# Performance work log

Measured on AMD Instinct MI355X. Metric: run time of the kernel, lower is better.

The kernel has to match this reference:

```python
import jax, jax.numpy as jnp
import numpy as np

B, T, D_Q, D_K, D_W = 128, 4096, 16, 16, 32


def setup_inputs() -> dict:
    key0 = jax.random.key(0)
    ks = jax.random.split(key0, 8)
    return {
        "query": jax.random.normal(ks[0], (B, 1, D_Q), dtype=jnp.float32),
        "key": jax.random.normal(ks[1], (B, T, D_K), dtype=jnp.float32),
        "value": jax.random.normal(ks[2], (B, T, D_K), dtype=jnp.float32),
        "W1": jax.random.normal(ks[3], (D_W, D_Q), dtype=jnp.float32) * 0.1,
        "W2": jax.random.normal(ks[4], (D_W, D_K), dtype=jnp.float32) * 0.1,
        "bias": jax.random.uniform(ks[5], (), dtype=jnp.float32, minval=-0.1, maxval=0.1),
        "v_w": jax.random.normal(ks[6], (1, D_W), dtype=jnp.float32) * 0.1,
        "v_b": jax.random.normal(ks[7], (1,), dtype=jnp.float32) * 0.1,
    }


def reference(query, key, value, W1, W2, bias, v_w, v_b):
    # Bahdanau additive attention.
    # query: [B,1,d_q], key/value: [B,T,d_k]
    q_proj = jnp.einsum('bqd,wd->bqw', query, W1)      # [B,1,d_w]
    k_proj = jnp.einsum('btd,wd->btw', key, W2)        # [B,T,d_w]
    h = jnp.tanh(k_proj + q_proj + bias)               # [B,T,d_w]
    score = (jnp.einsum('btw,ow->bto', h, v_w) + v_b).squeeze(-1)  # [B,T]
    attn = jax.nn.softmax(score, axis=-1)              # [B,T]
    context = jnp.einsum('bt,btd->bd', attn, value)[:, None, :]    # [B,1,d_v]
    return context, attn
```

## Files before the change

kernel.cpp:

```cpp
#include <hip/hip_runtime.h>

#define NB 128
#define NT 4096
#define DKD 16
#define DW 32
#define CHUNKS 4
#define TC 1024
#define BLK 256
#define PT 4

__device__ __forceinline__ float fast_tanh(float x) {
    float e = __expf(2.0f * x);
    return 1.0f - 2.0f * __builtin_amdgcn_rcpf(e + 1.0f);
}

__global__ __launch_bounds__(BLK, 2) void aa_score(
    const float* __restrict__ query, const float* __restrict__ key,
    const float* __restrict__ value, const float* __restrict__ W1,
    const float* __restrict__ W2, const float* __restrict__ bias,
    const float* __restrict__ v_w, const float* __restrict__ v_b,
    float* __restrict__ attn,
    float* __restrict__ ws_l,
    float* __restrict__ ws_ctx)
{
    const int b   = blockIdx.x >> 2;
    const int c   = blockIdx.x & (CHUNKS - 1);
    const int tid = threadIdx.x;

    __shared__ float2 s_cv[DW];
    __shared__ float s_rctx[4 * 16];
    __shared__ float s_rl[4];

    if (tid < DW) {
        float acc = bias[0];
        const float* q  = query + b * DKD;
        const float* wr = W1 + tid * DKD;
        #pragma unroll
        for (int d = 0; d < DKD; ++d) acc = fmaf(q[d], wr[d], acc);
        s_cv[tid] = make_float2(acc, v_w[tid]);
    }
    __syncthreads();

    const float vb = v_b[0];
    const size_t tbase = (size_t)b * NT + (size_t)c * TC + (size_t)tid * PT;
    const float4* kp = reinterpret_cast<const float4*>(key)   + tbase * 4;
    const float4* vp = reinterpret_cast<const float4*>(value) + tbase * 4;

    float4 k0[PT], k1[PT], k2[PT], k3[PT];
    float4 v0[PT], v1[PT], v2[PT], v3[PT];
    #pragma unroll
    for (int j = 0; j < PT; ++j) {
        k0[j] = kp[4*j + 0]; k1[j] = kp[4*j + 1];
        k2[j] = kp[4*j + 2]; k3[j] = kp[4*j + 3];
    }
    #pragma unroll
    for (int j = 0; j < PT; ++j) {
        v0[j] = vp[4*j + 0]; v1[j] = vp[4*j + 1];
        v2[j] = vp[4*j + 2]; v3[j] = vp[4*j + 3];
    }

    float sc[PT];
    #pragma unroll
    for (int j = 0; j < PT; ++j) sc[j] = vb;

    #pragma unroll 4
    for (int w = 0; w < DW; ++w) {
        const float4* wrow = reinterpret_cast<const float4*>(W2 + w * DKD);
        const float4 u0 = wrow[0], u1 = wrow[1], u2 = wrow[2], u3 = wrow[3];
        const float2 cv = s_cv[w];
        #pragma unroll
        for (int j = 0; j < PT; ++j) {
            float h = cv.x;
            h = fmaf(k0[j].x, u0.x, h); h = fmaf(k0[j].y, u0.y, h);
            h = fmaf(k0[j].z, u0.z, h); h = fmaf(k0[j].w, u0.w, h);
            h = fmaf(k1[j].x, u1.x, h); h = fmaf(k1[j].y, u1.y, h);
            h = fmaf(k1[j].z, u1.z, h); h = fmaf(k1[j].w, u1.w, h);
            h = fmaf(k2[j].x, u2.x, h); h = fmaf(k2[j].y, u2.y, h);
            h = fmaf(k2[j].z, u2.z, h); h = fmaf(k2[j].w, u2.w, h);
            h = fmaf(k3[j].x, u3.x, h); h = fmaf(k3[j].y, u3.y, h);
            h = fmaf(k3[j].z, u3.z, h); h = fmaf(k3[j].w, u3.w, h);
            sc[j] = fmaf(fast_tanh(h), cv.y, sc[j]);
        }
    }

    float l = 0.0f;
    float ctx[16];
    #pragma unroll
    for (int d = 0; d < 16; ++d) ctx[d] = 0.0f;

    float p[PT];
    #pragma unroll
    for (int j = 0; j < PT; ++j) {
        p[j] = __expf(sc[j]);
        l += p[j];
        ctx[ 0] = fmaf(p[j], v0[j].x, ctx[ 0]); ctx[ 1] = fmaf(p[j], v0[j].y, ctx[ 1]);
        ctx[ 2] = fmaf(p[j], v0[j].z, ctx[ 2]); ctx[ 3] = fmaf(p[j], v0[j].w, ctx[ 3]);
        ctx[ 4] = fmaf(p[j], v1[j].x, ctx[ 4]); ctx[ 5] = fmaf(p[j], v1[j].y, ctx[ 5]);
        ctx[ 6] = fmaf(p[j], v1[j].z, ctx[ 6]); ctx[ 7] = fmaf(p[j], v1[j].w, ctx[ 7]);
        ctx[ 8] = fmaf(p[j], v2[j].x, ctx[ 8]); ctx[ 9] = fmaf(p[j], v2[j].y, ctx[ 9]);
        ctx[10] = fmaf(p[j], v2[j].z, ctx[10]); ctx[11] = fmaf(p[j], v2[j].w, ctx[11]);
        ctx[12] = fmaf(p[j], v3[j].x, ctx[12]); ctx[13] = fmaf(p[j], v3[j].y, ctx[13]);
        ctx[14] = fmaf(p[j], v3[j].z, ctx[14]); ctx[15] = fmaf(p[j], v3[j].w, ctx[15]);
    }

    reinterpret_cast<float4*>(attn + (size_t)b * NT + (size_t)c * TC)[tid] =
        make_float4(p[0], p[1], p[2], p[3]);

    #pragma unroll
    for (int o = 32; o > 0; o >>= 1) l += __shfl_xor(l, o);
    #pragma unroll
    for (int d = 0; d < 16; ++d) {
        #pragma unroll
        for (int o = 32; o > 0; o >>= 1) ctx[d] += __shfl_xor(ctx[d], o);
    }
    const int wave = tid >> 6;
    const int lane = tid & 63;
    if (lane == 0) {
        s_rl[wave] = l;
        #pragma unroll
        for (int d = 0; d < 16; ++d) s_rctx[wave * 16 + d] = ctx[d];
    }
    __syncthreads();
    const int slot = b * CHUNKS + c;
    if (tid < 16)
        ws_ctx[slot * 16 + tid] =
            s_rctx[tid] + s_rctx[16 + tid] + s_rctx[32 + tid] + s_rctx[48 + tid];
    if (tid == 0)
        ws_l[slot] = s_rl[0] + s_rl[1] + s_rl[2] + s_rl[3];
}

__global__ __launch_bounds__(BLK) void aa_finish(
    float* __restrict__ out,
    const float* __restrict__ ws_l,
    const float* __restrict__ ws_ctx)
{
    const int b   = blockIdx.x >> 2;
    const int q   = blockIdx.x & 3;
    const int tid = threadIdx.x;

    float L = 0.0f;
    #pragma unroll
    for (int i = 0; i < CHUNKS; ++i) L += ws_l[b * CHUNKS + i];
    const float inv = 1.0f / L;

    float4* ap = reinterpret_cast<float4*>(out + NB * DKD + (size_t)b * NT) +
                 q * BLK + tid;
    float4 p = *ap;
    p.x *= inv; p.y *= inv; p.z *= inv; p.w *= inv;
    *ap = p;

    if (q == 0 && tid < DKD) {
        const float* wc = ws_ctx + b * CHUNKS * 16;
        float s = 0.0f;
        #pragma unroll
        for (int i = 0; i < CHUNKS; ++i) s += wc[i * 16 + tid];
        out[b * DKD + tid] = s * inv;
    }
}

extern "C" void kernel_launch(void* const* d_in, const int* in_sizes, int n_in,
                              void* d_out, int out_size, void* d_ws, size_t ws_size,
                              hipStream_t stream) {
    const float* query = (const float*)d_in[0];
    const float* key   = (const float*)d_in[1];
    const float* value = (const float*)d_in[2];
    const float* W1    = (const float*)d_in[3];
    const float* W2    = (const float*)d_in[4];
    const float* bias  = (const float*)d_in[5];
    const float* v_w   = (const float*)d_in[6];
    const float* v_b   = (const float*)d_in[7];
    float* out = (float*)d_out;

    float* ws_l   = (float*)d_ws;
    float* ws_ctx = ws_l + NB * CHUNKS;

    aa_score<<<NB * CHUNKS, BLK, 0, stream>>>(
        query, key, value, W1, W2, bias, v_w, v_b,
        out + NB * DKD, ws_l, ws_ctx);
    aa_finish<<<NB * (NT / 4 / BLK), BLK, 0, stream>>>(out, ws_l, ws_ctx);
}
```

Before: 122.0 us.

## Double-buffer key/value rows and process one timestep per stage

Replaces the upfront load of all four timesteps' key/value rows with a two-slot register double buffer. Each timestep is scored fully on its own, with the next slot's loads issued behind a sched_barrier, and the 16-term dot product is split into four partial sums to shorten the dependency chain. The aim is to cut register pressure and overlap global loads with tanh/FMA compute. In exchange, the four timesteps no longer share each W2 row load across an inner loop, so W2 rows are reloaded per timestep.

Measured after the change: 123.1 us. About the same (+0.9%).

```diff
diff --git a/kernel.cpp b/kernel.cpp
--- a/kernel.cpp
+++ b/kernel.cpp
@@ -13,6 +13,42 @@
     float e = __expf(2.0f * x);
     return 1.0f - 2.0f * __builtin_amdgcn_rcpf(e + 1.0f);
 }
+
+
+#define SCORE_STAGE(K0, K1, K2, K3, X0, X1, X2, X3, POUT)                     \
+    do {                                                                      \
+        float sc_ = vb;                                                       \
+        _Pragma("unroll 8")                                                   \
+        for (int w = 0; w < DW; ++w) {                                        \
+            const float4* wr_ = reinterpret_cast<const float4*>(W2) + w * 4;  \
+            const float4 u0 = wr_[0], u1 = wr_[1], u2 = wr_[2], u3 = wr_[3];  \
+            const float2 cv_ = s_cv[w];                                       \
+            float h0 = fmaf(K0.x, u0.x, cv_.x);                               \
+            h0 = fmaf(K0.y, u0.y, h0); h0 = fmaf(K0.z, u0.z, h0);             \
+            h0 = fmaf(K0.w, u0.w, h0);                                        \
+            float h1 = K1.x * u1.x;                                           \
+            h1 = fmaf(K1.y, u1.y, h1); h1 = fmaf(K1.z, u1.z, h1);             \
+            h1 = fmaf(K1.w, u1.w, h1);                                        \
+            float h2 = K2.x * u2.x;                                           \
+            h2 = fmaf(K2.y, u2.y, h2); h2 = fmaf(K2.z, u2.z, h2);             \
+            h2 = fmaf(K2.w, u2.w, h2);                                        \
+            float h3 = K3.x * u3.x;                                           \
+            h3 = fmaf(K3.y, u3.y, h3); h3 = fmaf(K3.z, u3.z, h3);             \
+            h3 = fmaf(K3.w, u3.w, h3);                                        \
+            const float h_ = (h0 + h1) + (h2 + h3);                           \
+            sc_ = fmaf(fast_tanh(h_), cv_.y, sc_);                            \
+        }                                                                     \
+        POUT = __expf(sc_);                                                   \
+        l += POUT;                                                            \
+        ctx[ 0] = fmaf(POUT, X0.x, ctx[ 0]); ctx[ 1] = fmaf(POUT, X0.y, ctx[ 1]); \
+        ctx[ 2] = fmaf(POUT, X0.z, ctx[ 2]); ctx[ 3] = fmaf(POUT, X0.w, ctx[ 3]); \
+        ctx[ 4] = fmaf(POUT, X1.x, ctx[ 4]); ctx[ 5] = fmaf(POUT, X1.y, ctx[ 5]); \
+        ctx[ 6] = fmaf(POUT, X1.z, ctx[ 6]); ctx[ 7] = fmaf(POUT, X1.w, ctx[ 7]); \
+        ctx[ 8] = fmaf(POUT, X2.x, ctx[ 8]); ctx[ 9] = fmaf(POUT, X2.y, ctx[ 9]); \
+        ctx[10] = fmaf(POUT, X2.z, ctx[10]); ctx[11] = fmaf(POUT, X2.w, ctx[11]); \
+        ctx[12] = fmaf(POUT, X3.x, ctx[12]); ctx[13] = fmaf(POUT, X3.y, ctx[13]); \
+        ctx[14] = fmaf(POUT, X3.z, ctx[14]); ctx[15] = fmaf(POUT, X3.w, ctx[15]); \
+    } while (0)
 
 __global__ __launch_bounds__(BLK, 2) void aa_score(
     const float* __restrict__ query, const float* __restrict__ key,
@@ -46,65 +82,34 @@
     const float4* kp = reinterpret_cast<const float4*>(key)   + tbase * 4;
     const float4* vp = reinterpret_cast<const float4*>(value) + tbase * 4;
 
-    float4 k0[PT], k1[PT], k2[PT], k3[PT];
-    float4 v0[PT], v1[PT], v2[PT], v3[PT];
-    #pragma unroll
-    for (int j = 0; j < PT; ++j) {
-        k0[j] = kp[4*j + 0]; k1[j] = kp[4*j + 1];
-        k2[j] = kp[4*j + 2]; k3[j] = kp[4*j + 3];
-    }
-    #pragma unroll
-    for (int j = 0; j < PT; ++j) {
-        v0[j] = vp[4*j + 0]; v1[j] = vp[4*j + 1];
-        v2[j] = vp[4*j + 2]; v3[j] = vp[4*j + 3];
-    }
-
-    float sc[PT];
-    #pragma unroll
-    for (int j = 0; j < PT; ++j) sc[j] = vb;
-
-    #pragma unroll 4
-    for (int w = 0; w < DW; ++w) {
-        const float4* wrow = reinterpret_cast<const float4*>(W2 + w * DKD);
-        const float4 u0 = wrow[0], u1 = wrow[1], u2 = wrow[2], u3 = wrow[3];
-        const float2 cv = s_cv[w];
-        #pragma unroll
-        for (int j = 0; j < PT; ++j) {
-            float h = cv.x;
-            h = fmaf(k0[j].x, u0.x, h); h = fmaf(k0[j].y, u0.y, h);
-            h = fmaf(k0[j].z, u0.z, h); h = fmaf(k0[j].w, u0.w, h);
-            h = fmaf(k1[j].x, u1.x, h); h = fmaf(k1[j].y, u1.y, h);
-            h = fmaf(k1[j].z, u1.z, h); h = fmaf(k1[j].w, u1.w, h);
-            h = fmaf(k2[j].x, u2.x, h); h = fmaf(k2[j].y, u2.y, h);
-            h = fmaf(k2[j].z, u2.z, h); h = fmaf(k2[j].w, u2.w, h);
-            h = fmaf(k3[j].x, u3.x, h); h = fmaf(k3[j].y, u3.y, h);
-            h = fmaf(k3[j].z, u3.z, h); h = fmaf(k3[j].w, u3.w, h);
-            sc[j] = fmaf(fast_tanh(h), cv.y, sc[j]);
-        }
-    }
-
     float l = 0.0f;
     float ctx[16];
     #pragma unroll
     for (int d = 0; d < 16; ++d) ctx[d] = 0.0f;
+    float p0, p1, p2, p3;
 
-    float p[PT];
-    #pragma unroll
-    for (int j = 0; j < PT; ++j) {
-        p[j] = __expf(sc[j]);
-        l += p[j];
-        ctx[ 0] = fmaf(p[j], v0[j].x, ctx[ 0]); ctx[ 1] = fmaf(p[j], v0[j].y, ctx[ 1]);
-        ctx[ 2] = fmaf(p[j], v0[j].z, ctx[ 2]); ctx[ 3] = fmaf(p[j], v0[j].w, ctx[ 3]);
-        ctx[ 4] = fmaf(p[j], v1[j].x, ctx[ 4]); ctx[ 5] = fmaf(p[j], v1[j].y, ctx[ 5]);
-        ctx[ 6] = fmaf(p[j], v1[j].z, ctx[ 6]); ctx[ 7] = fmaf(p[j], v1[j].w, ctx[ 7]);
-        ctx[ 8] = fmaf(p[j], v2[j].x, ctx[ 8]); ctx[ 9] = fmaf(p[j], v2[j].y, ctx[ 9]);
-        ctx[10] = fmaf(p[j], v2[j].z, ctx[10]); ctx[11] = fmaf(p[j], v2[j].w, ctx[11]);
-        ctx[12] = fmaf(p[j], v3[j].x, ctx[12]); ctx[13] = fmaf(p[j], v3[j].y, ctx[13]);
-        ctx[14] = fmaf(p[j], v3[j].z, ctx[14]); ctx[15] = fmaf(p[j], v3[j].w, ctx[15]);
-    }
+    float4 ka0 = kp[ 0], ka1 = kp[ 1], ka2 = kp[ 2], ka3 = kp[ 3];
+    float4 xa0 = vp[ 0], xa1 = vp[ 1], xa2 = vp[ 2], xa3 = vp[ 3];
+    float4 kb0 = kp[ 4], kb1 = kp[ 5], kb2 = kp[ 6], kb3 = kp[ 7];
+    float4 xb0 = vp[ 4], xb1 = vp[ 5], xb2 = vp[ 6], xb3 = vp[ 7];
+
+    SCORE_STAGE(ka0, ka1, ka2, ka3, xa0, xa1, xa2, xa3, p0);
+    __builtin_amdgcn_sched_barrier(0);
+    ka0 = kp[ 8]; ka1 = kp[ 9]; ka2 = kp[10]; ka3 = kp[11];
+    xa0 = vp[ 8]; xa1 = vp[ 9]; xa2 = vp[10]; xa3 = vp[11];
+
+    SCORE_STAGE(kb0, kb1, kb2, kb3, xb0, xb1, xb2, xb3, p1);
+    __builtin_amdgcn_sched_barrier(0);
+    kb0 = kp[12]; kb1 = kp[13]; kb2 = kp[14]; kb3 = kp[15];
+    xb0 = vp[12]; xb1 = vp[13]; xb2 = vp[14]; xb3 = vp[15];
+
+    SCORE_STAGE(ka0, ka1, ka2, ka3, xa0, xa1, xa2, xa3, p2);
+    __builtin_amdgcn_sched_barrier(0);
+
+    SCORE_STAGE(kb0, kb1, kb2, kb3, xb0, xb1, xb2, xb3, p3);
 
     reinterpret_cast<float4*>(attn + (size_t)b * NT + (size_t)c * TC)[tid] =
-        make_float4(p[0], p[1], p[2], p[3]);
+        make_float4(p0, p1, p2, p3);
 
     #pragma unroll
     for (int o = 32; o > 0; o >>= 1) l += __shfl_xor(l, o);
```
